# Kernel tuning notes

Measured on AMD Instinct MI355X. Metric: run time of the kernel, lower is better.

Reference implementation:

```python
import jax, jax.numpy as jnp
import numpy as np
from jax import lax

SCALE = 128.0        # x/y/w/h scale = model input size
MIN_SCORE = 0.5      # min_score_thresh
IOU_THRESH = 0.3     # mediapipe min_suppression_threshold
MAX_DET = 64         # fixed detection slots (jit-safe replacement for dynamic list)
NUM_ANCHORS = 896


def _decode(raw_boxes, anchors):
    # raw_boxes [B,A,16], anchors [A,4] = (x_center, y_center, w, h)
    ax, ay, aw, ah = anchors[:, 0], anchors[:, 1], anchors[:, 2], anchors[:, 3]
    xc = raw_boxes[..., 0] / SCALE * aw + ax
    yc = raw_boxes[..., 1] / SCALE * ah + ay
    w = raw_boxes[..., 2] / SCALE * aw
    h = raw_boxes[..., 3] / SCALE * ah
    box = jnp.stack([yc - h / 2, xc - w / 2, yc + h / 2, xc + w / 2], axis=-1)  # [B,A,4] ymin,xmin,ymax,xmax
    kp = raw_boxes[..., 4:16].reshape(*raw_boxes.shape[:-1], 6, 2)  # [B,A,6,2] (x,y)
    kpx = kp[..., 0] / SCALE * aw[:, None] + ax[:, None]
    kpy = kp[..., 1] / SCALE * ah[:, None] + ay[:, None]
    kps = jnp.stack([kpx, kpy], axis=-1).reshape(*raw_boxes.shape[:-1], 12)
    return jnp.concatenate([box, kps], axis=-1)  # [B,A,16]


def _iou(box, boxes):
    # box [4], boxes [A,4]; coords = ymin,xmin,ymax,xmax
    ymin = jnp.maximum(box[0], boxes[:, 0])
    xmin = jnp.maximum(box[1], boxes[:, 1])
    ymax = jnp.minimum(box[2], boxes[:, 2])
    xmax = jnp.minimum(box[3], boxes[:, 3])
    inter = jnp.maximum(ymax - ymin, 0.0) * jnp.maximum(xmax - xmin, 0.0)
    a1 = jnp.maximum(box[2] - box[0], 0.0) * jnp.maximum(box[3] - box[1], 0.0)
    a2 = jnp.maximum(boxes[:, 2] - boxes[:, 0], 0.0) * jnp.maximum(boxes[:, 3] - boxes[:, 1], 0.0)
    return inter / jnp.maximum(a1 + a2 - inter, 1e-6)


def _weighted_nms_single(coords, scores):
    # coords [A,16], scores [A] -> out [MAX_DET,17] sorted by descending score, zero-padded
    rem = jnp.where(scores >= MIN_SCORE, scores, -1.0)

    def step(rem, _):
        idx = jnp.argmax(rem)
        best = rem[idx]
        iou = _iou(coords[idx, :4], coords[:, :4])
        overlap = (iou > IOU_THRESH) & (rem > 0.0)
        wts = jnp.where(overlap, scores, 0.0)            # weight = candidate score
        denom = jnp.maximum(wts.sum(), 1e-6)
        blended = (coords * wts[:, None]).sum(0) / denom  # weighted box + keypoints
        det = jnp.concatenate([blended, best[None]])
        det = jnp.where(best > 0.0, det, jnp.zeros(17, det.dtype))
        rem = jnp.where(overlap, -1.0, rem)
        return rem, det

    _, out = lax.scan(step, rem, None, length=MAX_DET)
    return out


def _project(dets, matrix):
    # dets [B,MAX_DET,17], matrix [B,8] (first two rows of row-major 4x4 affine)
    m = matrix[:, None, :]  # [B,1,8]
    x_idx = jnp.array([1, 3, 4, 6, 8, 10, 12, 14])
    y_idx = jnp.array([0, 2, 5, 7, 9, 11, 13, 15])
    xs = dets[..., x_idx]
    ys = dets[..., y_idx]
    new_x = xs * m[..., 0:1] + ys * m[..., 1:2] + m[..., 3:4]
    new_y = xs * m[..., 4:5] + ys * m[..., 5:6] + m[..., 7:8]
    out = dets.at[..., x_idx].set(new_x)
    out = out.at[..., y_idx].set(new_y)
    # keep padded (invalid) rows zero, like the segmented-tensor original
    valid = dets[..., 16:17] > 0.0
    return jnp.where(valid, out, 0.0)


def _rescale(dets, h, w):
    hf = jnp.float32(h)
    wf = jnp.float32(w)
    scale = jnp.concatenate([
        jnp.array([1.0, 1.0]) * 0 + jnp.stack([hf, wf]),   # ymin*h, xmin*w
        jnp.stack([hf, wf]),                               # ymax*h, xmax*w
        jnp.tile(jnp.stack([wf, hf]), 6),                  # kp x*w, kp y*h
        jnp.ones((1,), jnp.float32),                       # score unchanged
    ])
    return dets * scale


def setup_inputs() -> dict:
    key = jax.random.key(0)
    k1, k2, k3, k4 = jax.random.split(key, 4)
    B = 2048
    return {
        "raw_boxes": jax.random.normal(k1, (B, NUM_ANCHORS, 16), jnp.float32),
        "raw_scores": jax.random.normal(k2, (B, NUM_ANCHORS), jnp.float32),
        "anchors": jax.random.uniform(k3, (NUM_ANCHORS, 4), jnp.float32),
        "transform_matrix": jax.random.normal(k4, (B, 8), jnp.float32),
        "h": 720,
        "w": 1280,
    }


def reference(raw_boxes, raw_scores, anchors, transform_matrix, h, w):
    coords = _decode(raw_boxes, anchors)                       # [B,A,16]
    scores = jax.nn.sigmoid(jnp.clip(raw_scores, -100.0, 100.0))
    dets = jax.vmap(_weighted_nms_single)(coords, scores)      # [B,MAX_DET,17]
    dets = _project(dets, transform_matrix)
    dets = _rescale(dets, h, w)
    return dets
```

## Files before the change

### kernel.cpp

```cpp
#include <hip/hip_runtime.h>
#include <math.h>

#define NANCH 896
#define MAXD 64
#define NS 14

__device__ __forceinline__ float selv17(const float d[17], int c) {
    float v = d[0];
#pragma unroll
    for (int k = 1; k < 17; ++k) v = (c == k) ? d[k] : v;
    return v;
}

__global__ __launch_bounds__(256, 2) void blaze_wave_kernel(
    const float* __restrict__ raw_boxes,
    const float* __restrict__ raw_scores,
    const float* __restrict__ anchors,
    const float* __restrict__ tmat,
    const int* __restrict__ hptr,
    const int* __restrict__ wptr,
    float* __restrict__ out,
    int B)
{
    const int lane = threadIdx.x & 63;
    const int wv   = threadIdx.x >> 6;
    const int b    = blockIdx.x * 4 + wv;
    if (b >= B) return;

    const float* rb = raw_boxes  + (size_t)b * (NANCH * 16);
    const float* rs = raw_scores + (size_t)b * NANCH;
    const float inv = 1.f / 128.f;

    float rem[NS], b0[NS], b1[NS], b2[NS], b3[NS];
#pragma unroll
    for (int j = 0; j < NS; ++j) {
        const int a = lane + 64 * j;
        float x = rs[a];
        x = fminf(fmaxf(x, -100.f), 100.f);
        float s = 1.f / (1.f + expf(-x));
        bool act = (s >= 0.5f);
        rem[j] = act ? s : -1.f;
        float t0 = 0.f, t1 = 0.f, t2 = 0.f, t3 = 0.f;
        if (act) {
            float4 an = *(const float4*)(anchors + a * 4);
            float4 r0 = *(const float4*)(rb + a * 16);
            float xc = r0.x * inv * an.z + an.x;
            float yc = r0.y * inv * an.w + an.y;
            float ww = r0.z * inv * an.z;
            float hh = r0.w * inv * an.w;
            t0 = yc - hh * 0.5f; t1 = xc - ww * 0.5f;
            t2 = yc + hh * 0.5f; t3 = xc + ww * 0.5f;
        }
        b0[j] = t0; b1[j] = t1; b2[j] = t2; b3[j] = t3;
    }

    const float* M = tmat + (size_t)b * 8;
    const float m0 = M[0], m1 = M[1], m3 = M[3];
    const float m4 = M[4], m5 = M[5], m7 = M[7];
    const float hf = (float)(*hptr);
    const float wf = (float)(*wptr);
    float* ob = out + (size_t)b * (MAXD * 17);

    int iter = 0;
    while (true) {
        float bv = -2.f; int bi = 1 << 30;
#pragma unroll
        for (int j = 0; j < NS; ++j) {
            if (rem[j] > bv) { bv = rem[j]; bi = lane + 64 * j; }
        }
#pragma unroll
        for (int s2 = 32; s2 >= 1; s2 >>= 1) {
            float ov = __shfl_xor(bv, s2, 64);
            int   oi = __shfl_xor(bi, s2, 64);
            if (ov > bv || (ov == bv && oi < bi)) { bv = ov; bi = oi; }
        }

        if (bv <= 0.f) {
            int n = (MAXD - iter) * 17;
            float* op = ob + iter * 17;
            for (int e = lane; e < n; e += 64) op[e] = 0.f;
            break;
        }

        const int bl = bi & 63, bj = bi >> 6;
        float vb0 = b0[0], vb1 = b1[0], vb2 = b2[0], vb3 = b3[0];
#pragma unroll
        for (int j = 1; j < NS; ++j) {
            if (bj == j) { vb0 = b0[j]; vb1 = b1[j]; vb2 = b2[j]; vb3 = b3[j]; }
        }
        const float bby0 = __shfl(vb0, bl, 64);
        const float bbx0 = __shfl(vb1, bl, 64);
        const float bby1 = __shfl(vb2, bl, 64);
        const float bbx1 = __shfl(vb3, bl, 64);
        const float a1 = fmaxf(bby1 - bby0, 0.f) * fmaxf(bbx1 - bbx0, 0.f);

        float acc[16];
#pragma unroll
        for (int c = 0; c < 16; ++c) acc[c] = 0.f;
        float wsum = 0.f;
        bool anyov = false;

#pragma unroll
        for (int j = 0; j < NS; ++j) {
            if (rem[j] > 0.f) {
                float ai = fmaxf(b2[j] - b0[j], 0.f) * fmaxf(b3[j] - b1[j], 0.f);
                float yA = fmaxf(bby0, b0[j]);
                float xA = fmaxf(bbx0, b1[j]);
                float yB = fminf(bby1, b2[j]);
                float xB = fminf(bbx1, b3[j]);
                float inter = fmaxf(yB - yA, 0.f) * fmaxf(xB - xA, 0.f);
                float iou = inter / fmaxf(a1 + ai - inter, 1e-6f);
                if (iou > 0.3f) {
                    anyov = true;
                    float wj = rem[j];
                    rem[j] = -1.f;
                    wsum += wj;
                    acc[0] += b0[j] * wj; acc[1] += b1[j] * wj;
                    acc[2] += b2[j] * wj; acc[3] += b3[j] * wj;
                    const int a = lane + 64 * j;
                    float4 an = *(const float4*)(anchors + a * 4);
                    const float* rp = rb + a * 16;
                    float4 r1 = *(const float4*)(rp + 4);
                    float4 r2 = *(const float4*)(rp + 8);
                    float4 r3 = *(const float4*)(rp + 12);
                    acc[4]  += (r1.x * inv * an.z + an.x) * wj;
                    acc[5]  += (r1.y * inv * an.w + an.y) * wj;
                    acc[6]  += (r1.z * inv * an.z + an.x) * wj;
                    acc[7]  += (r1.w * inv * an.w + an.y) * wj;
                    acc[8]  += (r2.x * inv * an.z + an.x) * wj;
                    acc[9]  += (r2.y * inv * an.w + an.y) * wj;
                    acc[10] += (r2.z * inv * an.z + an.x) * wj;
                    acc[11] += (r2.w * inv * an.w + an.y) * wj;
                    acc[12] += (r3.x * inv * an.z + an.x) * wj;
                    acc[13] += (r3.y * inv * an.w + an.y) * wj;
                    acc[14] += (r3.z * inv * an.z + an.x) * wj;
                    acc[15] += (r3.w * inv * an.w + an.y) * wj;
                }
            }
        }

        bool stuck = (__ballot(anyov) == 0ull);

        float det[17];
        if (!stuck) {
#pragma unroll
            for (int s2 = 32; s2 >= 1; s2 >>= 1) {
                wsum += __shfl_xor(wsum, s2, 64);
#pragma unroll
                for (int c = 0; c < 16; ++c) acc[c] += __shfl_xor(acc[c], s2, 64);
            }
            float dnm = fmaxf(wsum, 1e-6f);
#pragma unroll
            for (int c = 0; c < 16; ++c) det[c] = acc[c] / dnm;
        } else {
#pragma unroll
            for (int c = 0; c < 16; ++c) det[c] = 0.f;
        }
        det[16] = bv;

        {
            const int xi[8] = { 1, 3, 4, 6, 8, 10, 12, 14 };
            const int yi[8] = { 0, 2, 5, 7, 9, 11, 13, 15 };
#pragma unroll
            for (int k = 0; k < 8; ++k) {
                float x = det[xi[k]], y = det[yi[k]];
                det[xi[k]] = (x * m0 + y * m1 + m3) * wf;
                det[yi[k]] = (x * m4 + y * m5 + m7) * hf;
            }
        }

        if (stuck) {
            int n = (MAXD - iter) * 17;
            float* op = ob + iter * 17;
            for (int e = lane; e < n; e += 64) op[e] = selv17(det, e % 17);
            break;
        } else {
            if (lane < 17) ob[iter * 17 + lane] = selv17(det, lane);
            ++iter;
            if (iter == MAXD) break;
        }
    }
}

extern "C" void kernel_launch(void* const* d_in, const int* in_sizes, int n_in,
                              void* d_out, int out_size, void* d_ws, size_t ws_size,
                              hipStream_t stream) {
    (void)n_in; (void)out_size; (void)d_ws; (void)ws_size;
    const float* raw_boxes  = (const float*)d_in[0];
    const float* raw_scores = (const float*)d_in[1];
    const float* anchors    = (const float*)d_in[2];
    const float* tmat       = (const float*)d_in[3];
    const int*   hptr       = (const int*)d_in[4];
    const int*   wptr       = (const int*)d_in[5];
    float* out = (float*)d_out;

    const int B = in_sizes[0] / (NANCH * 16);
    blaze_wave_kernel<<<(B + 3) / 4, 256, 0, stream>>>(raw_boxes, raw_scores, anchors,
                                                       tmat, hptr, wptr, out, B);
}
```

Baseline: 208.4 us.

## Split box decode into a separate full-occupancy kernel writing workspace

```diff
diff --git a/kernel.cpp b/kernel.cpp
--- a/kernel.cpp
+++ b/kernel.cpp
@@ -12,9 +12,40 @@
     return v;
 }
 
-__global__ __launch_bounds__(256, 2) void blaze_wave_kernel(
+__global__ __launch_bounds__(256) void decode_kernel(
     const float* __restrict__ raw_boxes,
     const float* __restrict__ raw_scores,
+    const float* __restrict__ anchors,
+    float4* __restrict__ wsbox,
+    float*  __restrict__ wsrem,
+    int total)
+{
+    const int gr = blockIdx.x * 256 + threadIdx.x;
+    if (gr >= total) return;
+    const int a = gr % NANCH;
+    const float inv = 1.f / 128.f;
+
+    float x  = raw_scores[gr];
+    float4 r0 = *(const float4*)(raw_boxes + (size_t)gr * 16);
+    float4 an = *(const float4*)(anchors + a * 4);
+
+    x = fminf(fmaxf(x, -100.f), 100.f);
+    float s = 1.f / (1.f + expf(-x));
+
+    float xc = r0.x * inv * an.z + an.x;
+    float yc = r0.y * inv * an.w + an.y;
+    float ww = r0.z * inv * an.z;
+    float hh = r0.w * inv * an.w;
+
+    wsbox[gr] = make_float4(yc - hh * 0.5f, xc - ww * 0.5f,
+                            yc + hh * 0.5f, xc + ww * 0.5f);
+    wsrem[gr] = (s >= 0.5f) ? s : -1.f;
+}
+
+__global__ __launch_bounds__(256, 2) void nms_kernel(
+    const float4* __restrict__ wsbox,
+    const float*  __restrict__ wsrem,
+    const float* __restrict__ raw_boxes,
     const float* __restrict__ anchors,
     const float* __restrict__ tmat,
     const int* __restrict__ hptr,
@@ -27,31 +58,22 @@
     const int b    = blockIdx.x * 4 + wv;
     if (b >= B) return;
 
-    const float* rb = raw_boxes  + (size_t)b * (NANCH * 16);
-    const float* rs = raw_scores + (size_t)b * NANCH;
+    const float4* bx = wsbox + (size_t)b * NANCH;
+    const float*  rm = wsrem + (size_t)b * NANCH;
+    const float*  rb = raw_boxes + (size_t)b * (NANCH * 16);
     const float inv = 1.f / 128.f;
 
-    float rem[NS], b0[NS], b1[NS], b2[NS], b3[NS];
+    float4 bv4[NS];
+#pragma unroll
+    for (int j = 0; j < NS; ++j) bv4[j] = bx[lane + 64 * j];
+    float rem[NS];
+#pragma unroll
+    for (int j = 0; j < NS; ++j) rem[j] = rm[lane + 64 * j];
+
+    float b0[NS], b1[NS], b2[NS], b3[NS];
 #pragma unroll
     for (int j = 0; j < NS; ++j) {
-        const int a = lane + 64 * j;
-        float x = rs[a];
-        x = fminf(fmaxf(x, -100.f), 100.f);
-        float s = 1.f / (1.f + expf(-x));
-        bool act = (s >= 0.5f);
-        rem[j] = act ? s : -1.f;
-        float t0 = 0.f, t1 = 0.f, t2 = 0.f, t3 = 0.f;
-        if (act) {
-            float4 an = *(const float4*)(anchors + a * 4);
-            float4 r0 = *(const float4*)(rb + a * 16);
-            float xc = r0.x * inv * an.z + an.x;
-            float yc = r0.y * inv * an.w + an.y;
-            float ww = r0.z * inv * an.z;
-            float hh = r0.w * inv * an.w;
-            t0 = yc - hh * 0.5f; t1 = xc - ww * 0.5f;
-            t2 = yc + hh * 0.5f; t3 = xc + ww * 0.5f;
-        }
-        b0[j] = t0; b1[j] = t1; b2[j] = t2; b3[j] = t3;
+        b0[j] = bv4[j].x; b1[j] = bv4[j].y; b2[j] = bv4[j].z; b3[j] = bv4[j].w;
     }
 
     const float* M = tmat + (size_t)b * 8;
@@ -185,7 +207,7 @@
 extern "C" void kernel_launch(void* const* d_in, const int* in_sizes, int n_in,
                               void* d_out, int out_size, void* d_ws, size_t ws_size,
                               hipStream_t stream) {
-    (void)n_in; (void)out_size; (void)d_ws; (void)ws_size;
+    (void)n_in; (void)out_size; (void)ws_size;
     const float* raw_boxes  = (const float*)d_in[0];
     const float* raw_scores = (const float*)d_in[1];
     const float* anchors    = (const float*)d_in[2];
@@ -195,6 +217,14 @@
     float* out = (float*)d_out;
 
     const int B = in_sizes[0] / (NANCH * 16);
-    blaze_wave_kernel<<<(B + 3) / 4, 256, 0, stream>>>(raw_boxes, raw_scores, anchors,
-                                                       tmat, hptr, wptr, out, B);
-}
+    const int total = B * NANCH;
+
+    char* ws = (char*)d_ws;
+    float4* wsbox = (float4*)ws;
+    float*  wsrem = (float*)(ws + (size_t)total * 16);
+
+    decode_kernel<<<(total + 255) / 256, 256, 0, stream>>>(
+        raw_boxes, raw_scores, anchors, wsbox, wsrem, total);
+    nms_kernel<<<(B + 3) / 4, 256, 0, stream>>>(
+        wsbox, wsrem, raw_boxes, anchors, tmat, hptr, wptr, out, B);
+}
```

Result: slower. 223.5 us (+7.2%).
